# Kernel optimization log

Hardware: AMD Instinct MI355X
Metric: run time of the kernel (lower is better)

The kernel has to match this reference:

```python
import jax, jax.numpy as jnp
import numpy as np

D_MODEL = 1024
NUM_HEADS = 16
D_K = D_MODEL // NUM_HEADS
B, S = 4, 2048
NEG_INF = -1.0e9  # matches torch masked_fill value


def setup_inputs() -> dict:
    key = jax.random.key(0)
    ks = jax.random.split(key, 6)
    scale = 1.0 / np.sqrt(D_MODEL)
    x = jax.random.normal(ks[0], (B, S, D_MODEL), dtype=jnp.float32)
    # causal mask, broadcast over batch and heads: [1,1,S,S]
    mask = jnp.tril(jnp.ones((S, S), dtype=jnp.int32))[None, None]
    Wq = jax.random.normal(ks[1], (D_MODEL, D_MODEL), dtype=jnp.float32) * scale
    Wk = jax.random.normal(ks[2], (D_MODEL, D_MODEL), dtype=jnp.float32) * scale
    Wv = jax.random.normal(ks[3], (D_MODEL, D_MODEL), dtype=jnp.float32) * scale
    Wo = jax.random.normal(ks[4], (D_MODEL, D_MODEL), dtype=jnp.float32) * scale
    bq = jnp.zeros((D_MODEL,), jnp.float32)
    bk = jnp.zeros((D_MODEL,), jnp.float32)
    bv = jnp.zeros((D_MODEL,), jnp.float32)
    bo = jnp.zeros((D_MODEL,), jnp.float32)
    return {"x": x, "mask": mask, "Wq": Wq, "bq": bq, "Wk": Wk, "bk": bk,
            "Wv": Wv, "bv": bv, "Wo": Wo, "bo": bo}


def reference(x, mask, Wq, bq, Wk, bk, Wv, bv, Wo, bo):
    b, s, d = x.shape
    # projections (torch Linear: y = x @ W.T + b)
    q = (x @ Wq.T + bq).reshape(b, s, NUM_HEADS, D_K).transpose(0, 2, 1, 3)  # [B,H,S,Dk]
    k = (x @ Wk.T + bk).reshape(b, s, NUM_HEADS, D_K).transpose(0, 2, 1, 3)
    v = (x @ Wv.T + bv).reshape(b, s, NUM_HEADS, D_K).transpose(0, 2, 1, 3)
    scores = jnp.einsum("bhqd,bhkd->bhqk", q, k) / jnp.sqrt(jnp.float32(D_K))
    scores = jnp.where(mask == 0, NEG_INF, scores)
    attn = jax.nn.softmax(scores, axis=-1)
    out = jnp.einsum("bhqk,bhkd->bhqd", attn, v)  # [B,H,S,Dk]
    out = out.transpose(0, 2, 1, 3).reshape(b, s, d)
    return out @ Wo.T + bo
```

## Files before the change

kernel.cpp:

```cpp
#include <hip/hip_runtime.h>
#include <hip/hip_bf16.h>

#define D_MODEL 1024
#define NUM_HEADS 16
#define DK 64
#define BATCH 4
#define SEQ 2048

typedef __hip_bfloat16 bf16;
typedef __attribute__((ext_vector_type(8))) short bf16x8;
typedef __attribute__((ext_vector_type(4))) short bf16x4;
typedef __attribute__((ext_vector_type(4))) float f32x4;

typedef __attribute__((address_space(1))) const unsigned int gu32;
typedef __attribute__((address_space(3))) unsigned int lu32;

__device__ __forceinline__ void gll16(const bf16* g, bf16* l) {
    __builtin_amdgcn_global_load_lds((gu32*)g, (lu32*)l, 16, 0, 0);
}

__global__ __launch_bounds__(256)
void cvt_bf16(const float* __restrict__ x,  const float* __restrict__ Wq,
              const float* __restrict__ Wk, const float* __restrict__ Wv,
              const float* __restrict__ Wo, bf16* __restrict__ xb,
              bf16* __restrict__ Wb)
{
    size_t v = (size_t)blockIdx.x * 256 + threadIdx.x;
    size_t e = v * 4;
    const float* src; bf16* dst; size_t off;
    if (e < 8388608) { src = x; dst = xb; off = e; }
    else {
        size_t r = e - 8388608;
        int w = (int)(r >> 20);
        off = r & 1048575;
        src = (w == 0) ? Wq : (w == 1) ? Wk : (w == 2) ? Wv : Wo;
        dst = Wb + ((size_t)w << 20);
    }
    float4 f = *(const float4*)(src + off);
    bf16 o[4] = {__float2bfloat16(f.x), __float2bfloat16(f.y),
                 __float2bfloat16(f.z), __float2bfloat16(f.w)};
    *(bf16x4*)(dst + off) = *(const bf16x4*)o;
}

__device__ __forceinline__ void stage_gll(const bf16* __restrict__ src,
                                          bf16* lds, int t, int k0)
{
    #pragma unroll
    for (int p = 0; p < 4; ++p) {
        int idx = t + p * 256;
        int row = idx >> 3, cl = idx & 7;
        int cg = cl ^ (row & 7);
        gll16(src + (size_t)row * 1024 + k0 + cg * 8, lds + idx * 8);
    }
}

__device__ __forceinline__ bf16x8 frag_ld(const bf16* lds, int row, int h, int quad) {
    return *(const bf16x8*)(lds + row * 64 + (((h << 2) + quad) ^ (row & 7)) * 8);
}

__global__ __launch_bounds__(256)
void gemm_qkv(const bf16* __restrict__ xb, const bf16* __restrict__ Wb,
              const float* __restrict__ bq, const float* __restrict__ bk,
              const float* __restrict__ bv,
              bf16* __restrict__ Q, bf16* __restrict__ Kt, bf16* __restrict__ Vtr)
{
    __shared__ bf16 As[128 * 64];
    __shared__ bf16 Bs[128 * 64];
    const int t = threadIdx.x;
    const int wave = t >> 6, lane = t & 63;
    const int quad = lane >> 4, l16 = lane & 15;
    const int wr = wave >> 1, wc = wave & 1;
    const int proj = blockIdx.x >> 3;
    const int colBase = (blockIdx.x & 7) * 128;
    const int rowBase = blockIdx.y * 128;

    const bf16* Ablk = xb + (size_t)rowBase * 1024;
    const bf16* Bblk = Wb + ((size_t)proj << 20) + (size_t)colBase * 1024;
    const float* bias = proj == 0 ? bq : (proj == 1 ? bk : bv);

    f32x4 acc[4][4];
    #pragma unroll
    for (int i = 0; i < 4; ++i)
        #pragma unroll
        for (int j = 0; j < 4; ++j) acc[i][j] = (f32x4){0.f, 0.f, 0.f, 0.f};

    for (int k0 = 0; k0 < 1024; k0 += 64) {
        stage_gll(Ablk, As, t, k0);
        stage_gll(Bblk, Bs, t, k0);
        __syncthreads();
        #pragma unroll
        for (int h = 0; h < 2; ++h) {
            bf16x8 af[4], bfr[4];
            #pragma unroll
            for (int i = 0; i < 4; ++i)
                af[i] = frag_ld(As, wr * 64 + i * 16 + l16, h, quad);
            #pragma unroll
            for (int j = 0; j < 4; ++j)
                bfr[j] = frag_ld(Bs, wc * 64 + j * 16 + l16, h, quad);
            #pragma unroll
            for (int i = 0; i < 4; ++i)
                #pragma unroll
                for (int j = 0; j < 4; ++j)
                    acc[i][j] = __builtin_amdgcn_mfma_f32_16x16x32_bf16(af[i], bfr[j],
                                                                        acc[i][j], 0, 0, 0);
        }
        __syncthreads();
    }

    #pragma unroll
    for (int i = 0; i < 4; ++i)
        #pragma unroll
        for (int rr = 0; rr < 4; ++rr) {
            int r = rowBase + wr * 64 + i * 16 + quad * 4 + rr;
            int b_ = r >> 11, s_ = r & 2047;
            #pragma unroll
            for (int j = 0; j < 4; ++j) {
                int c = colBase + wc * 64 + j * 16 + l16;
                float v = acc[i][j][rr] + bias[c];
                int h_ = c >> 6, d_ = c & 63;
                size_t bh = (size_t)(b_ * NUM_HEADS + h_);
                if (proj == 2)
                    Vtr[(bh * DK + d_) * SEQ + s_] = __float2bfloat16(v);
                else {
                    bf16* dst = proj == 0 ? Q : Kt;
                    dst[(bh * SEQ + s_) * DK + d_] = __float2bfloat16(v);
                }
            }
        }
}

__global__ __launch_bounds__(256)
void gemm_out(const bf16* __restrict__ ctx, const bf16* __restrict__ Wb,
              const float* __restrict__ bo, float* __restrict__ out)
{
    __shared__ bf16 As[128 * 64];
    __shared__ bf16 Bs[128 * 64];
    const int t = threadIdx.x;
    const int wave = t >> 6, lane = t & 63;
    const int quad = lane >> 4, l16 = lane & 15;
    const int wr = wave >> 1, wc = wave & 1;
    const int colBase = blockIdx.x * 128;
    const int rowBase = blockIdx.y * 128;

    const bf16* Ablk = ctx + (size_t)rowBase * 1024;
    const bf16* Bblk = Wb + ((size_t)3 << 20) + (size_t)colBase * 1024;

    f32x4 acc[4][4];
    #pragma unroll
    for (int i = 0; i < 4; ++i)
        #pragma unroll
        for (int j = 0; j < 4; ++j) acc[i][j] = (f32x4){0.f, 0.f, 0.f, 0.f};

    for (int k0 = 0; k0 < 1024; k0 += 64) {
        stage_gll(Ablk, As, t, k0);
        stage_gll(Bblk, Bs, t, k0);
        __syncthreads();
        #pragma unroll
        for (int h = 0; h < 2; ++h) {
            bf16x8 af[4], bfr[4];
            #pragma unroll
            for (int i = 0; i < 4; ++i)
                af[i] = frag_ld(As, wr * 64 + i * 16 + l16, h, quad);
            #pragma unroll
            for (int j = 0; j < 4; ++j)
                bfr[j] = frag_ld(Bs, wc * 64 + j * 16 + l16, h, quad);
            #pragma unroll
            for (int i = 0; i < 4; ++i)
                #pragma unroll
                for (int j = 0; j < 4; ++j)
                    acc[i][j] = __builtin_amdgcn_mfma_f32_16x16x32_bf16(af[i], bfr[j],
                                                                        acc[i][j], 0, 0, 0);
        }
        __syncthreads();
    }

    #pragma unroll
    for (int i = 0; i < 4; ++i)
        #pragma unroll
        for (int rr = 0; rr < 4; ++rr) {
            int r = rowBase + wr * 64 + i * 16 + quad * 4 + rr;
            #pragma unroll
            for (int j = 0; j < 4; ++j) {
                int c = colBase + wc * 64 + j * 16 + l16;
                out[(size_t)r * 1024 + c] = acc[i][j][rr] + bo[c];
            }
        }
}

__global__ __launch_bounds__(256)
void attn_mfma(const bf16* __restrict__ Q, const bf16* __restrict__ K,
               const bf16* __restrict__ Vt, bf16* __restrict__ ctx)
{
    __shared__ bf16 Ks[128 * 64];
    __shared__ bf16 Vs[64 * 128];

    const int t    = threadIdx.x;
    const int wave = t >> 6, lane = t & 63;
    const int quad = lane >> 4, l16 = lane & 15;
    const int pair = blockIdx.x;
    const int bh   = blockIdx.y;
    const int b_ = bh >> 4, h_ = bh & 15;

    const bf16* Qb = Q  + (size_t)bh * SEQ * DK;
    const bf16* Kb = K  + (size_t)bh * SEQ * DK;
    const bf16* Vb = Vt + (size_t)bh * DK * SEQ;

    const float sc = 0.125f * 1.44269504089f;

    for (int phase = 0; phase < 2; ++phase) {
        const int qbi = phase ? (31 - pair) : pair;
        const int qb  = qbi * 64;
        const int qrow0 = qb + wave * 16;
        const int qlane = qrow0 + l16;

        bf16x8 qf0 = *(const bf16x8*)(Qb + (size_t)qlane * DK + quad * 8);
        bf16x8 qf1 = *(const bf16x8*)(Qb + (size_t)qlane * DK + 32 + quad * 8);

        f32x4 O[4];
        #pragma unroll
        for (int nc = 0; nc < 4; ++nc) O[nc] = (f32x4){0.f, 0.f, 0.f, 0.f};
        float lsum = 0.f;

        const int ntiles = (qbi >> 1) + 1;
        for (int kt = 0; kt < ntiles; ++kt) {
            const int k0 = kt * 128;
            #pragma unroll
            for (int p = 0; p < 4; ++p) {
                int idx = t + p * 256;
                int row = idx >> 3, cl = idx & 7;
                gll16(Kb + (size_t)(k0 + row) * DK + (cl ^ (row & 7)) * 8,
                      Ks + idx * 8);
            }
            #pragma unroll
            for (int p = 0; p < 4; ++p) {
                int idx = t + p * 256;
                int d = idx >> 4, c8 = idx & 15;
                gll16(Vb + (size_t)d * SEQ + k0 + (c8 ^ (d & 7)) * 8,
                      Vs + idx * 8);
            }
            __syncthreads();

            const bool need_mask = (kt == ntiles - 1);
            #pragma unroll
            for (int h = 0; h < 8; ++h) {
                bf16x8 kf0 = frag_ld(Ks, h * 16 + l16, 0, quad);
                bf16x8 kf1 = frag_ld(Ks, h * 16 + l16, 1, quad);
                f32x4 a = (f32x4){0.f, 0.f, 0.f, 0.f};
                a = __builtin_amdgcn_mfma_f32_16x16x32_bf16(kf0, qf0, a, 0, 0, 0);
                a = __builtin_amdgcn_mfma_f32_16x16x32_bf16(kf1, qf1, a, 0, 0, 0);
                bf16 pb[4];
                #pragma unroll
                for (int r = 0; r < 4; ++r) {
                    float p = exp2f(a[r] * sc - 32.0f);
                    int key = k0 + h * 16 + quad * 4 + r;
                    if (need_mask && key > qlane) p = 0.f;
                    lsum += p;
                    pb[r] = __float2bfloat16(p);
                }
                bf16x4 pa = *(const bf16x4*)pb;
                int lc = h * 2 + (quad >> 1);
                int c8 = (lc ^ (l16 & 7)) | (lc & 8);
                #pragma unroll
                for (int nc = 0; nc < 4; ++nc) {
                    int d = nc * 16 + l16;
                    bf16x4 vb = *(const bf16x4*)(Vs + d * 128 + c8 * 8 + (quad & 1) * 4);
                    O[nc] = __builtin_amdgcn_mfma_f32_16x16x16bf16_1k(pa, vb, O[nc],
                                                                      0, 0, 0);
                }
            }
            __syncthreads();
        }

        lsum += __shfl_xor(lsum, 16, 64);
        lsum += __shfl_xor(lsum, 32, 64);
        #pragma unroll
        for (int r = 0; r < 4; ++r) {
            float l_r = __shfl(lsum, quad * 4 + r, 64);
            float inv = 1.0f / l_r;
            int row = qrow0 + quad * 4 + r;
            #pragma unroll
            for (int nc = 0; nc < 4; ++nc) {
                float v = O[nc][r] * inv;
                ctx[((size_t)(b_ * SEQ + row)) * D_MODEL + h_ * DK + nc * 16 + l16] =
                    __float2bfloat16(v);
            }
        }
    }
}

extern "C" void kernel_launch(void* const* d_in, const int* in_sizes, int n_in,
                              void* d_out, int out_size, void* d_ws, size_t ws_size,
                              hipStream_t stream) {
    const float* x  = (const float*)d_in[0];
    const float* Wq = (const float*)d_in[2];
    const float* bq = (const float*)d_in[3];
    const float* Wk = (const float*)d_in[4];
    const float* bk = (const float*)d_in[5];
    const float* Wv = (const float*)d_in[6];
    const float* bv = (const float*)d_in[7];
    const float* Wo = (const float*)d_in[8];
    const float* bo = (const float*)d_in[9];
    float* out = (float*)d_out;

    const size_t per = (size_t)BATCH * NUM_HEADS * SEQ * DK;
    bf16* Q   = (bf16*)d_ws;
    bf16* Kt  = Q  + per;
    bf16* Vtr = Kt + per;
    bf16* xb  = Vtr + per;
    bf16* ctx = xb;
    bf16* Wb  = xb + per;

    hipLaunchKernelGGL(cvt_bf16, dim3(12288), dim3(256), 0, stream,
                       x, Wq, Wk, Wv, Wo, xb, Wb);

    hipLaunchKernelGGL(gemm_qkv, dim3(24, 64), dim3(256), 0, stream,
                       xb, Wb, bq, bk, bv, Q, Kt, Vtr);

    hipLaunchKernelGGL(attn_mfma, dim3(16, BATCH * NUM_HEADS), dim3(256), 0,
                       stream, Q, Kt, Vtr, ctx);

    hipLaunchKernelGGL(gemm_out, dim3(8, 64), dim3(256), 0, stream, ctx, Wb, bo, out);
}
```

Measured before the change: 323.5 us.

## Process two query row groups per wave to reuse K/V tiles in attention

The attention kernel now covers 128 query rows per block, with each wave handling two 16-row groups instead of one. Every K/V tile staged in LDS, and every V fragment loaded from it, now feeds twice as much MFMA work, which cuts global-to-LDS traffic and LDS reads per query. The grid is flattened to 512 blocks with the batch-head index varying fastest, which changes the scheduling order and likely L2 locality. In exchange there are half as many blocks and more accumulator registers per thread, which may lower occupancy and load balance.

```diff
diff --git a/kernel.cpp b/kernel.cpp
--- a/kernel.cpp
+++ b/kernel.cpp
@@ -197,8 +197,9 @@
     const int t    = threadIdx.x;
     const int wave = t >> 6, lane = t & 63;
     const int quad = lane >> 4, l16 = lane & 15;
-    const int pair = blockIdx.x;
-    const int bh   = blockIdx.y;
+    const int id   = blockIdx.x;
+    const int pair = id >> 6;
+    const int bh   = id & 63;
     const int b_ = bh >> 4, h_ = bh & 15;
 
     const bf16* Qb = Q  + (size_t)bh * SEQ * DK;
@@ -208,20 +209,26 @@
     const float sc = 0.125f * 1.44269504089f;
 
     for (int phase = 0; phase < 2; ++phase) {
-        const int qbi = phase ? (31 - pair) : pair;
-        const int qb  = qbi * 64;
-        const int qrow0 = qb + wave * 16;
-        const int qlane = qrow0 + l16;
-
-        bf16x8 qf0 = *(const bf16x8*)(Qb + (size_t)qlane * DK + quad * 8);
-        bf16x8 qf1 = *(const bf16x8*)(Qb + (size_t)qlane * DK + 32 + quad * 8);
-
-        f32x4 O[4];
-        #pragma unroll
-        for (int nc = 0; nc < 4; ++nc) O[nc] = (f32x4){0.f, 0.f, 0.f, 0.f};
-        float lsum = 0.f;
-
-        const int ntiles = (qbi >> 1) + 1;
+        const int qbi = phase ? (15 - pair) : pair;
+        const int qb  = qbi * 128;
+        const int qrow0 = qb + wave * 32;
+        bf16x8 qf[2][2];
+        int qlane[2];
+        #pragma unroll
+        for (int g = 0; g < 2; ++g) {
+            qlane[g] = qrow0 + g * 16 + l16;
+            qf[g][0] = *(const bf16x8*)(Qb + (size_t)qlane[g] * DK + quad * 8);
+            qf[g][1] = *(const bf16x8*)(Qb + (size_t)qlane[g] * DK + 32 + quad * 8);
+        }
+
+        f32x4 O[2][4];
+        #pragma unroll
+        for (int g = 0; g < 2; ++g)
+            #pragma unroll
+            for (int nc = 0; nc < 4; ++nc) O[g][nc] = (f32x4){0.f, 0.f, 0.f, 0.f};
+        float lsum[2] = {0.f, 0.f};
+
+        const int ntiles = qbi + 1;
         for (int kt = 0; kt < ntiles; ++kt) {
             const int k0 = kt * 128;
             #pragma unroll
@@ -245,44 +252,53 @@
             for (int h = 0; h < 8; ++h) {
                 bf16x8 kf0 = frag_ld(Ks, h * 16 + l16, 0, quad);
                 bf16x8 kf1 = frag_ld(Ks, h * 16 + l16, 1, quad);
-                f32x4 a = (f32x4){0.f, 0.f, 0.f, 0.f};
-                a = __builtin_amdgcn_mfma_f32_16x16x32_bf16(kf0, qf0, a, 0, 0, 0);
-                a = __builtin_amdgcn_mfma_f32_16x16x32_bf16(kf1, qf1, a, 0, 0, 0);
-                bf16 pb[4];
-                #pragma unroll
-                for (int r = 0; r < 4; ++r) {
-                    float p = exp2f(a[r] * sc - 32.0f);
-                    int key = k0 + h * 16 + quad * 4 + r;
-                    if (need_mask && key > qlane) p = 0.f;
-                    lsum += p;
-                    pb[r] = __float2bfloat16(p);
-                }
-                bf16x4 pa = *(const bf16x4*)pb;
                 int lc = h * 2 + (quad >> 1);
                 int c8 = (lc ^ (l16 & 7)) | (lc & 8);
+                bf16x4 vb[4];
                 #pragma unroll
                 for (int nc = 0; nc < 4; ++nc) {
                     int d = nc * 16 + l16;
-                    bf16x4 vb = *(const bf16x4*)(Vs + d * 128 + c8 * 8 + (quad & 1) * 4);
-                    O[nc] = __builtin_amdgcn_mfma_f32_16x16x16bf16_1k(pa, vb, O[nc],
-                                                                      0, 0, 0);
+                    vb[nc] = *(const bf16x4*)(Vs + d * 128 + c8 * 8 + (quad & 1) * 4);
                 }
+                #pragma unroll
+                for (int g = 0; g < 2; ++g) {
+                    f32x4 a = (f32x4){0.f, 0.f, 0.f, 0.f};
+                    a = __builtin_amdgcn_mfma_f32_16x16x32_bf16(kf0, qf[g][0], a, 0, 0, 0);
+                    a = __builtin_amdgcn_mfma_f32_16x16x32_bf16(kf1, qf[g][1], a, 0, 0, 0);
+                    bf16 pb[4];
+                    #pragma unroll
+                    for (int r = 0; r < 4; ++r) {
+                        float p = exp2f(a[r] * sc - 32.0f);
+                        int key = k0 + h * 16 + quad * 4 + r;
+                        if (need_mask && key > qlane[g]) p = 0.f;
+                        lsum[g] += p;
+                        pb[r] = __float2bfloat16(p);
+                    }
+                    bf16x4 pa = *(const bf16x4*)pb;
+                    #pragma unroll
+                    for (int nc = 0; nc < 4; ++nc)
+                        O[g][nc] = __builtin_amdgcn_mfma_f32_16x16x16bf16_1k(
+                            pa, vb[nc], O[g][nc], 0, 0, 0);
+                }
             }
             __syncthreads();
         }
 
-        lsum += __shfl_xor(lsum, 16, 64);
-        lsum += __shfl_xor(lsum, 32, 64);
-        #pragma unroll
-        for (int r = 0; r < 4; ++r) {
-            float l_r = __shfl(lsum, quad * 4 + r, 64);
-            float inv = 1.0f / l_r;
-            int row = qrow0 + quad * 4 + r;
-            #pragma unroll
-            for (int nc = 0; nc < 4; ++nc) {
-                float v = O[nc][r] * inv;
-                ctx[((size_t)(b_ * SEQ + row)) * D_MODEL + h_ * DK + nc * 16 + l16] =
-                    __float2bfloat16(v);
+        #pragma unroll
+        for (int g = 0; g < 2; ++g) {
+            lsum[g] += __shfl_xor(lsum[g], 16, 64);
+            lsum[g] += __shfl_xor(lsum[g], 32, 64);
+            #pragma unroll
+            for (int r = 0; r < 4; ++r) {
+                float l_r = __shfl(lsum[g], quad * 4 + r, 64);
+                float inv = 1.0f / l_r;
+                int row = qrow0 + g * 16 + quad * 4 + r;
+                #pragma unroll
+                for (int nc = 0; nc < 4; ++nc) {
+                    float v = O[g][nc][r] * inv;
+                    ctx[((size_t)(b_ * SEQ + row)) * D_MODEL + h_ * DK + nc * 16 + l16] =
+                        __float2bfloat16(v);
+                }
             }
         }
     }
@@ -316,7 +332,7 @@
     hipLaunchKernelGGL(gemm_qkv, dim3(24, 64), dim3(256), 0, stream,
                        xb, Wb, bq, bk, bv, Q, Kt, Vtr);
 
-    hipLaunchKernelGGL(attn_mfma, dim3(16, BATCH * NUM_HEADS), dim3(256), 0,
+    hipLaunchKernelGGL(attn_mfma, dim3(512), dim3(256), 0,
                        stream, Q, Kt, Vtr, ctx);
 
     hipLaunchKernelGGL(gemm_out, dim3(8, 64), dim3(256), 0, stream, ctx, Wb, bo, out);
```

After: 350.4 us. 1.08x slower.
